# Performance work log

Hardware: AMD Instinct MI355X
Metric: run time of the kernel (lower is better)

The kernel has to match this reference:

```python
import jax, jax.numpy as jnp
import numpy as np

DIM = 1024          # dim_feature
NUM_CLUSTERS = 8
N_PER = 4096        # patches per cluster (equal-size clusters)
NUM_SAMPLE = 1024   # num_sample_feature
QDIM = 128          # q projection dim
# sample_ratio = NUM_SAMPLE / (NUM_CLUSTERS*N_PER) = 1/32 -> top_k per cluster
TOPK = int(np.rint(N_PER * NUM_SAMPLE / (NUM_CLUSTERS * N_PER)))  # 128


def setup_inputs() -> dict:
    key = jax.random.key(0)
    ks = jax.random.split(key, 6)
    s = 1.0 / np.sqrt(DIM)
    return {
        "cluster_features": jax.random.normal(ks[0], (NUM_CLUSTERS, N_PER, DIM), jnp.float32),
        "key_feats": jax.random.normal(ks[1], (NUM_CLUSTERS, 1, DIM), jnp.float32),
        "q_w": jax.random.normal(ks[2], (QDIM, DIM), jnp.float32) * s,
        "q_b": jax.random.normal(ks[3], (QDIM,), jnp.float32) * 0.01,
        "v_w": jax.random.normal(ks[4], (DIM, DIM), jnp.float32) * s,
        "v_b": jax.random.normal(ks[5], (DIM,), jnp.float32) * 0.01,
    }


def reference(cluster_features, key_feats, q_w, q_b, v_w, v_b):
    scale_q = jnp.sqrt(jnp.float32(QDIM))

    def per_cluster(feats, key_feat):
        # NonLocalRanking with top_k=TOPK, top_fuse=False (adaptive path)
        Q = feats @ q_w.T + q_b            # [N, 128]
        qk = key_feat @ q_w.T + q_b        # [1, 128]
        A = (Q @ qk.T) / scale_q           # [N, 1]
        A = jax.nn.softmax(A, axis=0)      # softmax over patches (dim 0)
        _, idx = jax.lax.top_k(A[:, 0], TOPK)
        top_feats = feats[idx]             # [TOPK, DIM]
        V = feats @ v_w.T + v_b            # [N, DIM]
        fusion = (A.T @ V)[0]              # [DIM]
        return top_feats, fusion

    tops, fus = jax.vmap(per_cluster)(cluster_features, key_feats)
    selected = tops.reshape(-1, DIM)       # [NUM_CLUSTERS*TOPK, DIM] == [NUM_SAMPLE, DIM]
    # module pads/truncates to NUM_SAMPLE; here it is exactly NUM_SAMPLE
    selected = selected[:NUM_SAMPLE]
    return selected, fus
```

## Files before the change

### kernel.cpp

```cpp
#include <hip/hip_runtime.h>
#include <math.h>


#define DIM   1024
#define NC    8
#define NPER  4096
#define QD    128
#define TOPK  128
#define K1B   128

typedef unsigned long long u64;
typedef __attribute__((ext_vector_type(2))) unsigned long long ull2;

__global__ __launch_bounds__(256) void k0_prep(
    const float* __restrict__ key_feats, const float* __restrict__ q_w,
    const float* __restrict__ q_b, float* __restrict__ w_all)
{
    const int c  = blockIdx.x >> 2, jc = blockIdx.x & 3;
    const int tid = threadIdx.x;
    __shared__ float part[256];
    __shared__ float qs[QD];

    {
        const int k = tid >> 1, half = tid & 1;
        const float4* qr4 = (const float4*)(q_w + (size_t)k * DIM + half * 512);
        const float4* kf4 = (const float4*)(key_feats + (size_t)c * DIM + half * 512);
        float s = 0.f;
        #pragma unroll 16
        for (int j = 0; j < 128; ++j) {
            float4 a = qr4[j], b = kf4[j];
            s += a.x*b.x + a.y*b.y + a.z*b.z + a.w*b.w;
        }
        part[tid] = s;
    }
    __syncthreads();
    if (tid < QD) qs[tid] = part[2*tid] + part[2*tid+1] + q_b[tid];
    __syncthreads();

    const int j = jc * 256 + tid;
    float s = 0.f;
    #pragma unroll 16
    for (int k = 0; k < QD; ++k)
        s += q_w[(size_t)k * DIM + j] * qs[k];
    w_all[c * DIM + j] = s * 0.08838834764831845f;
}

__global__ __launch_bounds__(256, 4) void k1_main(
    const float* __restrict__ feats, const float* __restrict__ w_all,
    u64* __restrict__ keys,
    float* __restrict__ pacc,
    float* __restrict__ pm, float* __restrict__ pz)
{
    const int c    = blockIdx.y;
    const int blk  = blockIdx.x;
    const int tid  = threadIdx.x;
    const int lane = tid & 63;
    const int wave = tid >> 6;

    const float4* w4 = (const float4*)(w_all + c * DIM);
    float4 wv[4];
    #pragma unroll
    for (int q = 0; q < 4; ++q) wv[q] = w4[lane + 64*q];

    float4 acc[4];
    #pragma unroll
    for (int q = 0; q < 4; ++q) acc[q] = make_float4(0.f, 0.f, 0.f, 0.f);
    float m = -INFINITY, Z = 0.f;

    const int wslot = blk * 4 + wave;
    const float* fc = feats + (size_t)c * NPER * DIM;

    float4 fA[4], fB[4];
    {
        const float4* f4 = (const float4*)(fc + (size_t)wslot * DIM);
        #pragma unroll
        for (int q = 0; q < 4; ++q) fA[q] = f4[lane + 64*q];
    }

    #define K1_PROCESS(FREG, ROW)                                              \
    do {                                                                       \
        float p = 0.f;                                                         \
        _Pragma("unroll")                                                      \
        for (int q = 0; q < 4; ++q)                                            \
            p += FREG[q].x*wv[q].x + FREG[q].y*wv[q].y +                       \
                 FREG[q].z*wv[q].z + FREG[q].w*wv[q].w;                        \
        _Pragma("unroll")                                                      \
        for (int off = 32; off > 0; off >>= 1) p += __shfl_xor(p, off, 64);    \
        if (lane == 0) {                                                       \
            unsigned int b = __float_as_uint(p);                               \
            unsigned int u = b ^ ((b & 0x80000000u) ? 0xFFFFFFFFu : 0x80000000u); \
            keys[c * NPER + (ROW)] = ((u64)u << 32) | (unsigned int)(~(ROW));  \
        }                                                                      \
        if (p > m) {                  \
            const float sOld = __expf(m - p);                                  \
            Z = Z * sOld + 1.f;                                                \
            _Pragma("unroll")                                                  \
            for (int q = 0; q < 4; ++q) {                                      \
                acc[q].x = acc[q].x * sOld + FREG[q].x;                        \
                acc[q].y = acc[q].y * sOld + FREG[q].y;                        \
                acc[q].z = acc[q].z * sOld + FREG[q].z;                        \
                acc[q].w = acc[q].w * sOld + FREG[q].w;                        \
            }                                                                  \
            m = p;                                                             \
        } else {                                                               \
            const float t = __expf(p - m);                                     \
            Z += t;                                                            \
            _Pragma("unroll")                                                  \
            for (int q = 0; q < 4; ++q) {                                      \
                acc[q].x += t * FREG[q].x;                                     \
                acc[q].y += t * FREG[q].y;                                     \
                acc[q].z += t * FREG[q].z;                                     \
                acc[q].w += t * FREG[q].w;                                     \
            }                                                                  \
        }                                                                      \
    } while (0)

    for (int it = 0; it < 8; it += 2) {
        const int r0 = wslot + 512 * it;
        {
            const float4* f4 = (const float4*)(fc + (size_t)(r0 + 512) * DIM);
            #pragma unroll
            for (int q = 0; q < 4; ++q) fB[q] = f4[lane + 64*q];
        }
        K1_PROCESS(fA, r0);
        if (it + 2 < 8) {
            const float4* f4 = (const float4*)(fc + (size_t)(r0 + 1024) * DIM);
            #pragma unroll
            for (int q = 0; q < 4; ++q) fA[q] = f4[lane + 64*q];
        }
        K1_PROCESS(fB, r0 + 512);
    }
    #undef K1_PROCESS

    __shared__ float sm[4], sz[4];
    __shared__ float sacc[4][DIM];
    if (lane == 0) { sm[wave] = m; sz[wave] = Z; }
    #pragma unroll
    for (int q = 0; q < 4; ++q)
        ((float4*)sacc[wave])[lane + 64*q] = acc[q];
    __syncthreads();

    const float mb = fmaxf(fmaxf(sm[0], sm[1]), fmaxf(sm[2], sm[3]));
    const float e0 = __expf(sm[0] - mb), e1 = __expf(sm[1] - mb);
    const float e2 = __expf(sm[2] - mb), e3 = __expf(sm[3] - mb);
    float4 a0 = ((float4*)sacc[0])[tid];
    float4 a1 = ((float4*)sacc[1])[tid];
    float4 a2 = ((float4*)sacc[2])[tid];
    float4 a3 = ((float4*)sacc[3])[tid];
    float4 o;
    o.x = a0.x*e0 + a1.x*e1 + a2.x*e2 + a3.x*e3;
    o.y = a0.y*e0 + a1.y*e1 + a2.y*e2 + a3.y*e3;
    o.z = a0.z*e0 + a1.z*e1 + a2.z*e2 + a3.z*e3;
    o.w = a0.w*e0 + a1.w*e1 + a2.w*e2 + a3.w*e3;
    ((float4*)(pacc + (size_t)(c * K1B + blk) * DIM))[tid] = o;
    if (tid == 0) {
        pm[c * K1B + blk] = mb;
        pz[c * K1B + blk] = sz[0]*e0 + sz[1]*e1 + sz[2]*e2 + sz[3]*e3;
    }
}

__global__ __launch_bounds__(256) void k2_combine(
    const float* __restrict__ pacc, const float* __restrict__ pm,
    const float* __restrict__ pz, float* __restrict__ g)
{
    const int c = blockIdx.y, jb = blockIdx.x;
    const int tid  = threadIdx.x;
    const int slot = tid & 63;
    const int bg   = tid >> 6;
    __shared__ float spm[K1B], spz[K1B], swe[K1B];
    __shared__ float szc;
    __shared__ float4 sred[3][64];

    if (tid < K1B) spm[tid] = pm[c*K1B + tid];
    else spz[tid - K1B] = pz[c*K1B + tid - K1B];
    __syncthreads();
    float mc = -INFINITY;
    for (int b = 0; b < K1B; ++b) mc = fmaxf(mc, spm[b]);
    if (tid < K1B) swe[tid] = __expf(spm[tid] - mc);
    __syncthreads();
    if (tid == 0) {
        float z = 0.f;
        for (int b = 0; b < K1B; ++b) z += spz[b] * swe[b];
        szc = z;
    }

    const int jbase = jb * 256 + slot * 4;
    float4 a = make_float4(0.f, 0.f, 0.f, 0.f);
    #pragma unroll
    for (int k = 0; k < 32; ++k) {
        const int b = bg * 32 + k;
        const float e = swe[b];
        float4 v = *(const float4*)(pacc + (size_t)(c*K1B + b) * DIM + jbase);
        a.x += e*v.x; a.y += e*v.y; a.z += e*v.z; a.w += e*v.w;
    }
    if (bg) sred[bg-1][slot] = a;
    __syncthreads();
    if (bg == 0) {
        float4 t0 = sred[0][slot], t1 = sred[1][slot], t2 = sred[2][slot];
        const float inv = 1.0f / szc;
        float4 o;
        o.x = (a.x + t0.x + t1.x + t2.x) * inv;
        o.y = (a.y + t0.y + t1.y + t2.y) * inv;
        o.z = (a.z + t0.z + t1.z + t2.z) * inv;
        o.w = (a.w + t0.w + t1.w + t2.w) * inv;
        *(float4*)(g + c * DIM + jbase) = o;
    }
}

__global__ __launch_bounds__(256) void k3a_rank(
    const u64* __restrict__ keys, int* __restrict__ part)
{
    const int iblk = blockIdx.x, js = blockIdx.y, c = blockIdx.z;
    const int tid = threadIdx.x;
    __shared__ u64 lk[512];
    ((float4*)lk)[tid] = ((const float4*)(keys + c * NPER + js * 512))[tid];

    const int ibase = iblk * 1024;
    u64 ki[4];
    #pragma unroll
    for (int q = 0; q < 4; ++q) ki[q] = keys[c * NPER + ibase + tid + 256*q];
    __syncthreads();

    int cnt0 = 0, cnt1 = 0, cnt2 = 0, cnt3 = 0;
    const ull2* lk2 = (const ull2*)lk;
    #pragma unroll 4
    for (int jt = 0; jt < 256; ++jt) {
        ull2 kj = lk2[jt];
        cnt0 += (kj.x > ki[0]) + (kj.y > ki[0]);
        cnt1 += (kj.x > ki[1]) + (kj.y > ki[1]);
        cnt2 += (kj.x > ki[2]) + (kj.y > ki[2]);
        cnt3 += (kj.x > ki[3]) + (kj.y > ki[3]);
    }
    int* dst = part + ((js * NC + c) << 12) + ibase + tid;
    dst[0]   = cnt0; dst[256] = cnt1; dst[512] = cnt2; dst[768] = cnt3;
}

__global__ __launch_bounds__(256) void k3b_gather(
    const int* __restrict__ part, const float* __restrict__ feats,
    float* __restrict__ out_sel)
{
    const int c = blockIdx.y;
    const int i = blockIdx.x * 256 + threadIdx.x;
    const int tid = threadIdx.x;
    __shared__ int list_i[TOPK], list_r[TOPK];
    __shared__ int cnt;
    if (tid == 0) cnt = 0;
    __syncthreads();

    int r = 0;
    #pragma unroll
    for (int js = 0; js < 8; ++js) r += part[((js * NC + c) << 12) + i];
    if (r < TOPK) {
        const int s = atomicAdd(&cnt, 1);
        list_i[s] = i; list_r[s] = r;
    }
    __syncthreads();

    const int n = cnt;
    for (int s = 0; s < n; ++s) {
        const float4* src = (const float4*)(feats + ((size_t)c * NPER + list_i[s]) * DIM);
        float4* dst = (float4*)(out_sel + ((size_t)c * TOPK + list_r[s]) * DIM);
        dst[tid] = src[tid];
    }
}

__global__ __launch_bounds__(256) void k5_fusion(
    const float* __restrict__ v_w, const float* __restrict__ v_b,
    const float* __restrict__ g, float* __restrict__ fus)
{
    __shared__ float4 sg[NC][256];
    const int tid = threadIdx.x, lane = tid & 63, wave = tid >> 6;
    for (int t = tid; t < NC * 256; t += 256)
        ((float4*)sg)[t] = ((const float4*)g)[t];
    __syncthreads();

    const int row0 = blockIdx.x * 8 + wave * 2;
    for (int rr = 0; rr < 2; ++rr) {
        const int o = row0 + rr;
        const float4* vr = (const float4*)(v_w + (size_t)o * DIM);
        float4 v[4];
        #pragma unroll
        for (int u = 0; u < 4; ++u) v[u] = vr[lane + 64*u];
        float p[NC];
        #pragma unroll
        for (int cc = 0; cc < NC; ++cc) {
            float s = 0.f;
            #pragma unroll
            for (int u = 0; u < 4; ++u) {
                float4 gv = sg[cc][lane + 64*u];
                s += v[u].x*gv.x + v[u].y*gv.y + v[u].z*gv.z + v[u].w*gv.w;
            }
            p[cc] = s;
        }
        #pragma unroll
        for (int off = 32; off > 0; off >>= 1) {
            #pragma unroll
            for (int cc = 0; cc < NC; ++cc) p[cc] += __shfl_xor(p[cc], off, 64);
        }
        if (lane == 0) {
            const float b = v_b[o];
            #pragma unroll
            for (int cc = 0; cc < NC; ++cc) fus[cc * DIM + o] = p[cc] + b;
        }
    }
}

extern "C" void kernel_launch(void* const* d_in, const int* in_sizes, int n_in,
                              void* d_out, int out_size, void* d_ws, size_t ws_size,
                              hipStream_t stream) {
    const float* feats     = (const float*)d_in[0];
    const float* key_feats = (const float*)d_in[1];
    const float* q_w       = (const float*)d_in[2];
    const float* q_b       = (const float*)d_in[3];
    const float* v_w       = (const float*)d_in[4];
    const float* v_b       = (const float*)d_in[5];
    float* out      = (float*)d_out;
    float* out_sel  = out;
    float* out_fus  = out + (size_t)1024 * 1024;

    u64*   keys   = (u64*)d_ws;
    float* pacc   = (float*)(keys + NC * NPER);
    float* pm     = pacc + (size_t)NC * K1B * DIM;
    float* pz     = pm + NC * K1B;
    float* g      = pz + NC * K1B;
    float* w_all  = g + NC * DIM;
    int*   part   = (int*)(w_all + NC * DIM);

    k0_prep    <<<dim3(NC * 4),    256, 0, stream>>>(key_feats, q_w, q_b, w_all);
    k1_main    <<<dim3(K1B, NC),   256, 0, stream>>>(feats, w_all, keys, pacc, pm, pz);
    k2_combine <<<dim3(4, NC),     256, 0, stream>>>(pacc, pm, pz, g);
    k3a_rank   <<<dim3(4, 8, NC),  256, 0, stream>>>(keys, part);
    k3b_gather <<<dim3(16, NC),    256, 0, stream>>>(part, feats, out_sel);
    k5_fusion  <<<dim3(128),       256, 0, stream>>>(v_w, v_b, g, out_fus);
}
```

Measured before the change: 257.3 us.

## Merge independent combine/rank and gather/fusion kernels into two fat launches

Combines k2_combine and k3a_rank into one launch that dispatches on block index, and k3b_gather and k5_fusion into a second, cutting launches from six to four. Each pair of independent stages can now run concurrently on the GPU. The rank stage's key split is also doubled to 16 chunks of 256, giving more blocks with less work each, at the cost of 16 partial counts summed per element in the gather. The shared-memory footprint per block is now the union of both branches.

```diff
diff --git a/kernel.cpp b/kernel.cpp
--- a/kernel.cpp
+++ b/kernel.cpp
@@ -8,6 +8,7 @@
 #define QD    128
 #define TOPK  128
 #define K1B   128
+#define JS    16
 
 typedef unsigned long long u64;
 typedef __attribute__((ext_vector_type(2))) unsigned long long ull2;
@@ -159,148 +160,147 @@
     }
 }
 
-__global__ __launch_bounds__(256) void k2_combine(
+__global__ __launch_bounds__(256) void fat_a(
     const float* __restrict__ pacc, const float* __restrict__ pm,
-    const float* __restrict__ pz, float* __restrict__ g)
-{
-    const int c = blockIdx.y, jb = blockIdx.x;
-    const int tid  = threadIdx.x;
-    const int slot = tid & 63;
-    const int bg   = tid >> 6;
-    __shared__ float spm[K1B], spz[K1B], swe[K1B];
-    __shared__ float szc;
-    __shared__ float4 sred[3][64];
-
-    if (tid < K1B) spm[tid] = pm[c*K1B + tid];
-    else spz[tid - K1B] = pz[c*K1B + tid - K1B];
-    __syncthreads();
-    float mc = -INFINITY;
-    for (int b = 0; b < K1B; ++b) mc = fmaxf(mc, spm[b]);
-    if (tid < K1B) swe[tid] = __expf(spm[tid] - mc);
-    __syncthreads();
-    if (tid == 0) {
-        float z = 0.f;
-        for (int b = 0; b < K1B; ++b) z += spz[b] * swe[b];
-        szc = z;
-    }
-
-    const int jbase = jb * 256 + slot * 4;
-    float4 a = make_float4(0.f, 0.f, 0.f, 0.f);
-    #pragma unroll
-    for (int k = 0; k < 32; ++k) {
-        const int b = bg * 32 + k;
-        const float e = swe[b];
-        float4 v = *(const float4*)(pacc + (size_t)(c*K1B + b) * DIM + jbase);
-        a.x += e*v.x; a.y += e*v.y; a.z += e*v.z; a.w += e*v.w;
-    }
-    if (bg) sred[bg-1][slot] = a;
-    __syncthreads();
-    if (bg == 0) {
-        float4 t0 = sred[0][slot], t1 = sred[1][slot], t2 = sred[2][slot];
-        const float inv = 1.0f / szc;
-        float4 o;
-        o.x = (a.x + t0.x + t1.x + t2.x) * inv;
-        o.y = (a.y + t0.y + t1.y + t2.y) * inv;
-        o.z = (a.z + t0.z + t1.z + t2.z) * inv;
-        o.w = (a.w + t0.w + t1.w + t2.w) * inv;
-        *(float4*)(g + c * DIM + jbase) = o;
-    }
-}
-
-__global__ __launch_bounds__(256) void k3a_rank(
+    const float* __restrict__ pz, float* __restrict__ g,
     const u64* __restrict__ keys, int* __restrict__ part)
 {
-    const int iblk = blockIdx.x, js = blockIdx.y, c = blockIdx.z;
     const int tid = threadIdx.x;
-    __shared__ u64 lk[512];
-    ((float4*)lk)[tid] = ((const float4*)(keys + c * NPER + js * 512))[tid];
-
-    const int ibase = iblk * 1024;
-    u64 ki[4];
-    #pragma unroll
-    for (int q = 0; q < 4; ++q) ki[q] = keys[c * NPER + ibase + tid + 256*q];
-    __syncthreads();
-
-    int cnt0 = 0, cnt1 = 0, cnt2 = 0, cnt3 = 0;
-    const ull2* lk2 = (const ull2*)lk;
-    #pragma unroll 4
-    for (int jt = 0; jt < 256; ++jt) {
-        ull2 kj = lk2[jt];
-        cnt0 += (kj.x > ki[0]) + (kj.y > ki[0]);
-        cnt1 += (kj.x > ki[1]) + (kj.y > ki[1]);
-        cnt2 += (kj.x > ki[2]) + (kj.y > ki[2]);
-        cnt3 += (kj.x > ki[3]) + (kj.y > ki[3]);
-    }
-    int* dst = part + ((js * NC + c) << 12) + ibase + tid;
-    dst[0]   = cnt0; dst[256] = cnt1; dst[512] = cnt2; dst[768] = cnt3;
-}
-
-__global__ __launch_bounds__(256) void k3b_gather(
+    if (blockIdx.x < 32) {
+        const int c = blockIdx.x >> 2, jb = blockIdx.x & 3;
+        const int slot = tid & 63;
+        const int bg   = tid >> 6;
+        __shared__ float spm[K1B], spz[K1B], swe[K1B];
+        __shared__ float szc;
+        __shared__ float4 sred[3][64];
+
+        if (tid < K1B) spm[tid] = pm[c*K1B + tid];
+        else spz[tid - K1B] = pz[c*K1B + tid - K1B];
+        __syncthreads();
+        float mc = -INFINITY;
+        for (int b = 0; b < K1B; ++b) mc = fmaxf(mc, spm[b]);
+        if (tid < K1B) swe[tid] = __expf(spm[tid] - mc);
+        __syncthreads();
+        if (tid == 0) {
+            float z = 0.f;
+            for (int b = 0; b < K1B; ++b) z += spz[b] * swe[b];
+            szc = z;
+        }
+
+        const int jbase = jb * 256 + slot * 4;
+        float4 a = make_float4(0.f, 0.f, 0.f, 0.f);
+        #pragma unroll
+        for (int k = 0; k < 32; ++k) {
+            const int b = bg * 32 + k;
+            const float e = swe[b];
+            float4 v = *(const float4*)(pacc + (size_t)(c*K1B + b) * DIM + jbase);
+            a.x += e*v.x; a.y += e*v.y; a.z += e*v.z; a.w += e*v.w;
+        }
+        if (bg) sred[bg-1][slot] = a;
+        __syncthreads();
+        if (bg == 0) {
+            float4 t0 = sred[0][slot], t1 = sred[1][slot], t2 = sred[2][slot];
+            const float inv = 1.0f / szc;
+            float4 o;
+            o.x = (a.x + t0.x + t1.x + t2.x) * inv;
+            o.y = (a.y + t0.y + t1.y + t2.y) * inv;
+            o.z = (a.z + t0.z + t1.z + t2.z) * inv;
+            o.w = (a.w + t0.w + t1.w + t2.w) * inv;
+            *(float4*)(g + c * DIM + jbase) = o;
+        }
+    } else {
+        const int t = blockIdx.x - 32;
+        const int iblk = t & 3, js = (t >> 2) & (JS-1), c = t >> 6;
+        __shared__ u64 lk[256];
+        if (tid < 128)
+            ((float4*)lk)[tid] = ((const float4*)(keys + c * NPER + js * 256))[tid];
+
+        const int ibase = iblk * 1024;
+        u64 ki[4];
+        #pragma unroll
+        for (int q = 0; q < 4; ++q) ki[q] = keys[c * NPER + ibase + tid + 256*q];
+        __syncthreads();
+
+        int cnt0 = 0, cnt1 = 0, cnt2 = 0, cnt3 = 0;
+        const ull2* lk2 = (const ull2*)lk;
+        #pragma unroll 4
+        for (int jt = 0; jt < 128; ++jt) {
+            ull2 kj = lk2[jt];
+            cnt0 += (kj.x > ki[0]) + (kj.y > ki[0]);
+            cnt1 += (kj.x > ki[1]) + (kj.y > ki[1]);
+            cnt2 += (kj.x > ki[2]) + (kj.y > ki[2]);
+            cnt3 += (kj.x > ki[3]) + (kj.y > ki[3]);
+        }
+        int* dst = part + ((js * NC + c) << 12) + ibase + tid;
+        dst[0]   = cnt0; dst[256] = cnt1; dst[512] = cnt2; dst[768] = cnt3;
+    }
+}
+
+__global__ __launch_bounds__(256) void fat_b(
     const int* __restrict__ part, const float* __restrict__ feats,
-    float* __restrict__ out_sel)
-{
-    const int c = blockIdx.y;
-    const int i = blockIdx.x * 256 + threadIdx.x;
-    const int tid = threadIdx.x;
-    __shared__ int list_i[TOPK], list_r[TOPK];
-    __shared__ int cnt;
-    if (tid == 0) cnt = 0;
-    __syncthreads();
-
-    int r = 0;
-    #pragma unroll
-    for (int js = 0; js < 8; ++js) r += part[((js * NC + c) << 12) + i];
-    if (r < TOPK) {
-        const int s = atomicAdd(&cnt, 1);
-        list_i[s] = i; list_r[s] = r;
-    }
-    __syncthreads();
-
-    const int n = cnt;
-    for (int s = 0; s < n; ++s) {
-        const float4* src = (const float4*)(feats + ((size_t)c * NPER + list_i[s]) * DIM);
-        float4* dst = (float4*)(out_sel + ((size_t)c * TOPK + list_r[s]) * DIM);
-        dst[tid] = src[tid];
-    }
-}
-
-__global__ __launch_bounds__(256) void k5_fusion(
+    float* __restrict__ out_sel,
     const float* __restrict__ v_w, const float* __restrict__ v_b,
     const float* __restrict__ g, float* __restrict__ fus)
 {
-    __shared__ float4 sg[NC][256];
-    const int tid = threadIdx.x, lane = tid & 63, wave = tid >> 6;
-    for (int t = tid; t < NC * 256; t += 256)
-        ((float4*)sg)[t] = ((const float4*)g)[t];
-    __syncthreads();
-
-    const int row0 = blockIdx.x * 8 + wave * 2;
-    for (int rr = 0; rr < 2; ++rr) {
-        const int o = row0 + rr;
-        const float4* vr = (const float4*)(v_w + (size_t)o * DIM);
-        float4 v[4];
+    const int tid = threadIdx.x;
+    if (blockIdx.x < 128) {
+        const int c = blockIdx.x >> 4;
+        const int i = (blockIdx.x & 15) * 256 + tid;
+        __shared__ int list_i[TOPK], list_r[TOPK];
+        __shared__ int cnt;
+        if (tid == 0) cnt = 0;
+        __syncthreads();
+
+        int r = 0;
         #pragma unroll
-        for (int u = 0; u < 4; ++u) v[u] = vr[lane + 64*u];
-        float p[NC];
-        #pragma unroll
-        for (int cc = 0; cc < NC; ++cc) {
-            float s = 0.f;
-            #pragma unroll
-            for (int u = 0; u < 4; ++u) {
-                float4 gv = sg[cc][lane + 64*u];
-                s += v[u].x*gv.x + v[u].y*gv.y + v[u].z*gv.z + v[u].w*gv.w;
+        for (int js = 0; js < JS; ++js) r += part[((js * NC + c) << 12) + i];
+        if (r < TOPK) {
+            const int s = atomicAdd(&cnt, 1);
+            list_i[s] = i; list_r[s] = r;
+        }
+        __syncthreads();
+
+        const int n = cnt;
+        for (int s = 0; s < n; ++s) {
+            const float4* src = (const float4*)(feats + ((size_t)c * NPER + list_i[s]) * DIM);
+            float4* dst = (float4*)(out_sel + ((size_t)c * TOPK + list_r[s]) * DIM);
+            dst[tid] = src[tid];
+        }
+    } else {
+        __shared__ float4 sg[NC][256];
+        const int lane = tid & 63, wave = tid >> 6;
+        for (int t = tid; t < NC * 256; t += 256)
+            ((float4*)sg)[t] = ((const float4*)g)[t];
+        __syncthreads();
+
+        const int row0 = (blockIdx.x - 128) * 8 + wave * 2;
+        for (int rr = 0; rr < 2; ++rr) {
+            const int o = row0 + rr;
+            const float4* vr = (const float4*)(v_w + (size_t)o * DIM);
+            float4 v[4];
+            #pragma unroll
+            for (int u = 0; u < 4; ++u) v[u] = vr[lane + 64*u];
+            float p[NC];
+            #pragma unroll
+            for (int cc = 0; cc < NC; ++cc) {
+                float s = 0.f;
+                #pragma unroll
+                for (int u = 0; u < 4; ++u) {
+                    float4 gv = sg[cc][lane + 64*u];
+                    s += v[u].x*gv.x + v[u].y*gv.y + v[u].z*gv.z + v[u].w*gv.w;
+                }
+                p[cc] = s;
             }
-            p[cc] = s;
-        }
-        #pragma unroll
-        for (int off = 32; off > 0; off >>= 1) {
-            #pragma unroll
-            for (int cc = 0; cc < NC; ++cc) p[cc] += __shfl_xor(p[cc], off, 64);
-        }
-        if (lane == 0) {
-            const float b = v_b[o];
-            #pragma unroll
-            for (int cc = 0; cc < NC; ++cc) fus[cc * DIM + o] = p[cc] + b;
+            #pragma unroll
+            for (int off = 32; off > 0; off >>= 1) {
+                #pragma unroll
+                for (int cc = 0; cc < NC; ++cc) p[cc] += __shfl_xor(p[cc], off, 64);
+            }
+            if (lane == 0) {
+                const float b = v_b[o];
+                #pragma unroll
+                for (int cc = 0; cc < NC; ++cc) fus[cc * DIM + o] = p[cc] + b;
+            }
         }
     }
 }
@@ -326,10 +326,8 @@
     float* w_all  = g + NC * DIM;
     int*   part   = (int*)(w_all + NC * DIM);
 
-    k0_prep    <<<dim3(NC * 4),    256, 0, stream>>>(key_feats, q_w, q_b, w_all);
-    k1_main    <<<dim3(K1B, NC),   256, 0, stream>>>(feats, w_all, keys, pacc, pm, pz);
-    k2_combine <<<dim3(4, NC),     256, 0, stream>>>(pacc, pm, pz, g);
-    k3a_rank   <<<dim3(4, 8, NC),  256, 0, stream>>>(keys, part);
-    k3b_gather <<<dim3(16, NC),    256, 0, stream>>>(part, feats, out_sel);
-    k5_fusion  <<<dim3(128),       256, 0, stream>>>(v_w, v_b, g, out_fus);
-}
+    k0_prep <<<dim3(NC * 4),       256, 0, stream>>>(key_feats, q_w, q_b, w_all);
+    k1_main <<<dim3(K1B, NC),      256, 0, stream>>>(feats, w_all, keys, pacc, pm, pz);
+    fat_a   <<<dim3(32 + 4*JS*NC), 256, 0, stream>>>(pacc, pm, pz, g, keys, part);
+    fat_b   <<<dim3(256),          256, 0, stream>>>(part, feats, out_sel, v_w, v_b, g, out_fus);
+}
```

New measurement: 246.1 us. -4.4%, faster.
